# Performance work log

Hardware: AMD Instinct MI355X
Metric: run time of the kernel (lower is better)

The kernel has to match this reference:

```python
import jax, jax.numpy as jnp
import numpy as np

B, N, DIM = 2, 2048, 1024
H, DH = 16, 64
DIM_INNER = H * DH
EPS = float(jnp.finfo(jnp.float32).eps)  # torch nn.RMSNorm default eps = finfo.eps
THETA = 10000.0


def setup_inputs() -> dict:
    key = jax.random.key(0)
    ks = jax.random.split(key, 6)
    s = 0.02
    tokens = jax.random.normal(ks[0], (B, N, DIM), dtype=jnp.float32)
    w_norm = jnp.ones((DIM,), jnp.float32)                      # prenorm RMSNorm weight
    w_q = jax.random.normal(ks[1], (DIM, DIM_INNER), jnp.float32) * s
    w_k = jax.random.normal(ks[2], (DIM, 3 * DIM_INNER), jnp.float32) * s
    w_v = jax.random.normal(ks[3], (DIM, 3 * DIM_INNER), jnp.float32) * s
    w_key_norms = jnp.ones((3, DH), jnp.float32)                # 3 key RMSNorms
    w_nested_knorm = jnp.ones((DH,), jnp.float32)
    w_out = jax.random.normal(ks[4], (DIM_INNER, DIM), jnp.float32) * s
    return {"tokens": tokens, "w_norm": w_norm, "w_q": w_q, "w_k": w_k,
            "w_v": w_v, "w_key_norms": w_key_norms,
            "w_nested_knorm": w_nested_knorm, "w_out": w_out}


def rmsnorm(x, w):
    var = jnp.mean(jnp.square(x), axis=-1, keepdims=True)
    return x * jax.lax.rsqrt(var + EPS) * w


def rope(x):
    # interleaved (GPT-J style) rotary, as in rotary_embedding_torch defaults
    n, d = x.shape[-2], x.shape[-1]
    inv_freq = 1.0 / (THETA ** (jnp.arange(0, d, 2, dtype=jnp.float32) / d))
    freqs = jnp.arange(n, dtype=jnp.float32)[:, None] * inv_freq   # (n, d/2)
    cos = jnp.repeat(jnp.cos(freqs), 2, axis=-1)                   # (n, d)
    sin = jnp.repeat(jnp.sin(freqs), 2, axis=-1)
    x1, x2 = x[..., ::2], x[..., 1::2]
    x_rot = jnp.stack((-x2, x1), axis=-1).reshape(x.shape)         # rotate_half
    return x * cos + x_rot * sin


def attend(q, k, v):
    # rotate_queries_with_cached_keys with equal lengths -> plain rotary on both
    q = rope(q)
    k = rope(k)
    d = q.shape[-1]
    scores = jnp.einsum('bhqd,bhkd->bhqk', q, k) / jnp.sqrt(jnp.float32(d))
    n = scores.shape[-1]
    causal = jnp.tril(jnp.ones((n, n), dtype=bool))
    scores = jnp.where(causal, scores, -jnp.inf)
    attn = jax.nn.softmax(scores, axis=-1)
    return jnp.einsum('bhqk,bhkd->bhqd', attn, v)


def reference(tokens, w_norm, w_q, w_k, w_v, w_key_norms, w_nested_knorm, w_out):
    b, n = tokens.shape[:2]
    x = rmsnorm(tokens, w_norm)                                    # prenorm
    q = (x @ w_q).reshape(b, n, H, DH).transpose(0, 2, 1, 3)       # (b,h,n,d)
    # chunk(3, dim=-1) then split heads -> (3,b,h,n,d)
    ks = (x @ w_k).reshape(b, n, 3, H, DH).transpose(2, 0, 3, 1, 4)
    vs = (x @ w_v).reshape(b, n, 3, H, DH).transpose(2, 0, 3, 1, 4)
    ks = rmsnorm(ks, w_key_norms[:, None, None, None, :])          # per-branch key norm
    # three parallel causal attentions sharing the same queries
    nq, nk, nv = jax.vmap(attend, in_axes=(None, 0, 0))(q, ks, vs)
    nk = rmsnorm(nk, w_nested_knorm)
    out = attend(nq, nk, nv)                                       # nested attention
    out = out.transpose(0, 2, 1, 3).reshape(b, n, DIM_INNER)       # merge heads
    return out @ w_out
```

## Files before the change

kernel.cpp:

```cpp
#include <hip/hip_runtime.h>
#include <hip/hip_bf16.h>
#include <stdint.h>

typedef unsigned short u16;
typedef __attribute__((ext_vector_type(8))) short short8;
typedef __attribute__((ext_vector_type(4))) float float4v;
typedef __attribute__((ext_vector_type(4))) unsigned int uint4v;

#define B_    2
#define N_    2048
#define DIM_  1024
#define H_    16
#define DH_   64
#define DI_   1024
#define EPS_  1.1920928955078125e-07f
#define LOG2_THETA 13.287712379549449f
#define SCL_  0.18033688011112042f

__device__ __forceinline__ float bf2f(u16 u) {
    union { unsigned int i; float f; } v; v.i = ((unsigned int)u) << 16; return v.f;
}
__device__ __forceinline__ u16 f2bf(float f) {
    union { float f; unsigned int i; } v; v.f = f;
    unsigned int r = v.i + 0x7fff + ((v.i >> 16) & 1);
    return (u16)(r >> 16);
}
__device__ __forceinline__ unsigned int cvtpk(float a, float b) {
    unsigned int r;
    asm("v_cvt_pk_bf16_f32 %0, %1, %2" : "=v"(r) : "v"(a), "v"(b));
    return r;
}
__device__ __forceinline__ int perm32(int n) {
    return (n & ~31) + (((n >> 2) & 3) * 8) + (((n >> 4) & 1) * 4) + (n & 3);
}

__global__ __launch_bounds__(256) void k_pre(
    const float* __restrict__ w_q, const float* __restrict__ w_k,
    const float* __restrict__ w_v, u16* __restrict__ dstW,
    const float* __restrict__ tok, const float* __restrict__ w_norm,
    u16* __restrict__ xn) {
    int bx = blockIdx.x;
    int t = threadIdx.x;
    __shared__ float tile[32][33];
    __shared__ float red[4];
    if (bx < 7168) {
        int c0 = (bx % 224) * 32, k0 = (bx / 224) * 32;
        const float* src; int sN, sc0;
        if (c0 < 1024)      { src = w_q; sN = 1024; sc0 = c0; }
        else if (c0 < 4096) { src = w_k; sN = 3072; sc0 = c0 - 1024; }
        else                { src = w_v; sN = 3072; sc0 = c0 - 4096; }
        int tx = t & 31, ty = t >> 5;
#pragma unroll
        for (int i = 0; i < 4; ++i)
            tile[ty + 8 * i][tx] = src[(size_t)(k0 + ty + 8 * i) * sN + sc0 + tx];
        __syncthreads();
#pragma unroll
        for (int i = 0; i < 4; ++i)
            dstW[(size_t)(c0 + ty + 8 * i) * 1024 + k0 + tx] = f2bf(tile[tx][ty + 8 * i]);
    } else {
        int row = bx - 7168;
        const float* tr = tok + (size_t)row * DIM_ + t * 4;
        float4v v = *(const float4v*)tr;
        float ss = v[0] * v[0] + v[1] * v[1] + v[2] * v[2] + v[3] * v[3];
#pragma unroll
        for (int o = 32; o; o >>= 1) ss += __shfl_xor(ss, o, 64);
        if ((t & 63) == 0) red[t >> 6] = ss;
        __syncthreads();
        ss = red[0] + red[1] + red[2] + red[3];
        float rs = rsqrtf(ss * (1.0f / DIM_) + EPS_);
        const float* wp = w_norm + t * 4;
        uint2 pk;
        pk.x = cvtpk(v[0] * rs * wp[0], v[1] * rs * wp[1]);
        pk.y = cvtpk(v[2] * rs * wp[2], v[3] * rs * wp[3]);
        *(uint2*)(xn + (size_t)row * DIM_ + t * 4) = pk;
    }
}

__global__ __launch_bounds__(256) void k_transpose(
    const float* __restrict__ src, u16* __restrict__ dst, int K, int N) {
    __shared__ float tile[32][33];
    int n0 = blockIdx.x * 32, k0 = blockIdx.y * 32;
    int tx = threadIdx.x, ty = threadIdx.y;
#pragma unroll
    for (int i = 0; i < 4; ++i)
        tile[ty + 8 * i][tx] = src[(size_t)(k0 + ty + 8 * i) * N + n0 + tx];
    __syncthreads();
#pragma unroll
    for (int i = 0; i < 4; ++i)
        dst[(size_t)(n0 + ty + 8 * i) * K + k0 + tx] = f2bf(tile[tx][ty + 8 * i]);
}

__global__ __launch_bounds__(256) void k_post1(
    u16* __restrict__ QKVB, u16* __restrict__ Vt, const float* __restrict__ w) {
    int bx = blockIdx.x;
    int t = threadIdx.x;
    __shared__ u16 tile[64][72];
    if (bx < 3072) {
        int y = bx >> 5;
        int s = y >> 5;
        int b = (y >> 4) & 1;
        int h = y & 15;
        int n0 = (bx & 31) * 64;
#pragma unroll
        for (int i = 0; i < 2; ++i) {
            int idx = i * 256 + t;
            int row = idx >> 3, c = idx & 7;
            uint4v v = *(const uint4v*)(QKVB + ((size_t)(b * N_) + n0 + row) * 7168
                                            + 4096 + s * 1024 + h * 64 + c * 8);
            *(uint4v*)&tile[row][c * 8] = v;
        }
        __syncthreads();
        u16* out = Vt + (size_t)y * 64 * N_;
#pragma unroll
        for (int i = 0; i < 2; ++i) {
            int idx = i * 256 + t;
            int dh = idx >> 3, og = idx & 7;
            u16 vals[8];
#pragma unroll
            for (int j = 0; j < 8; ++j) {
                int m = og * 8 + j;
                int nn = (m & 32) + (m & 3) + ((m >> 3) & 3) * 4 + ((m >> 2) & 1) * 16;
                vals[j] = tile[nn][dh];
            }
            *(uint4v*)(out + (size_t)dh * N_ + n0 + og * 8) = *(const uint4v*)vals;
        }
    } else {
        int wid = (bx - 3072) * 4 + (t >> 6);
        int lane = t & 63;
        int r8 = lane >> 3, e8 = lane & 7;
        int hg = wid & 1;
        int s = (wid >> 1) % 3;
        int row = wid / 6;
        int n = row & (N_ - 1);
        int h = hg * 8 + r8;
        u16* p = QKVB + (size_t)row * 7168 + 1024 + s * 1024 + h * 64 + e8 * 8;
        uint4v v = *(const uint4v*)p;
        float x[8];
#pragma unroll
        for (int j = 0; j < 8; ++j) x[j] = bf2f(((const u16*)&v)[j]);
        float ss = 0.f;
#pragma unroll
        for (int j = 0; j < 8; ++j) ss += x[j] * x[j];
        ss += __shfl_xor(ss, 1, 64);
        ss += __shfl_xor(ss, 2, 64);
        ss += __shfl_xor(ss, 4, 64);
        float rs = rsqrtf(ss * (1.0f / 64.0f) + EPS_);
        const float* ws = w + s * 64 + e8 * 8;
        uint4v pk;
#pragma unroll
        for (int tp = 0; tp < 4; ++tp) {
            int d0 = e8 * 8 + 2 * tp;
            float xn0 = x[2 * tp] * rs * ws[2 * tp];
            float xn1 = x[2 * tp + 1] * rs * ws[2 * tp + 1];
            float inv = exp2f(-(float)d0 * (LOG2_THETA / 64.0f));
            float fr = (float)n * inv;
            float sv, cv;
            __sincosf(fr, &sv, &cv);
            pk[tp] = cvtpk(xn0 * cv - xn1 * sv, xn1 * cv + xn0 * sv);
        }
        *(uint4v*)p = pk;
    }
}

template <bool OUT_F32>
__global__ __launch_bounds__(256) void k_gemm_bt(
    const u16* __restrict__ A, const u16* __restrict__ Bt, void* __restrict__ Cv,
    int K, int Ncols) {
    __shared__ u16 As[2][128 * 32];
    __shared__ u16 Bs[2][128 * 32];
    int m0 = blockIdx.x * 128, n0 = blockIdx.y * 128;
    int t = threadIdx.x;
    int w = t >> 6, lane = t & 63, ln = lane & 15, quad = lane >> 4;
    int wm = w & 1, wn = w >> 1;
    float4v acc[4][4] = {};
    const u16* Ag = A + (size_t)m0 * K;
    const u16* Bg = Bt + (size_t)n0 * K;

    auto stage = [&](int k0, int buf) {
#pragma unroll
        for (int i = 0; i < 2; ++i) {
            int idx = i * 256 + t;
            int row = idx >> 2, kb = idx & 3;
            int csrc = (kb ^ ((row >> 1) & 3)) * 8;
            const u16* ga = Ag + (size_t)row * K + k0 + csrc;
            const u16* gb = Bg + (size_t)row * K + k0 + csrc;
            __builtin_amdgcn_global_load_lds(
                (const __attribute__((address_space(1))) void*)ga,
                (__attribute__((address_space(3))) void*)(As[buf] + idx * 8), 16, 0, 0);
            __builtin_amdgcn_global_load_lds(
                (const __attribute__((address_space(1))) void*)gb,
                (__attribute__((address_space(3))) void*)(Bs[buf] + idx * 8), 16, 0, 0);
        }
    };

    int nk = K >> 5;
    stage(0, 0);
    int rchunk = (quad ^ ((ln >> 1) & 3)) * 8;

    for (int kt = 0; kt < nk; ++kt) {
        asm volatile("s_waitcnt vmcnt(0)" ::: "memory");
        __syncthreads();
        if (kt + 1 < nk) stage((kt + 1) << 5, (kt + 1) & 1);
        int buf = kt & 1;
        short8 af[4], bfr[4];
#pragma unroll
        for (int mt = 0; mt < 4; ++mt)
            af[mt] = *(const short8*)(As[buf] + (wm * 64 + mt * 16 + ln) * 32 + rchunk);
#pragma unroll
        for (int nt = 0; nt < 4; ++nt)
            bfr[nt] = *(const short8*)(Bs[buf] + (wn * 64 + nt * 16 + ln) * 32 + rchunk);
#pragma unroll
        for (int mt = 0; mt < 4; ++mt)
#pragma unroll
            for (int nt = 0; nt < 4; ++nt)
                acc[mt][nt] = __builtin_amdgcn_mfma_f32_16x16x32_bf16(
                    af[mt], bfr[nt], acc[mt][nt], 0, 0, 0);
    }
#pragma unroll
    for (int mt = 0; mt < 4; ++mt)
#pragma unroll
        for (int nt = 0; nt < 4; ++nt)
#pragma unroll
            for (int r = 0; r < 4; ++r) {
                int row = m0 + wm * 64 + mt * 16 + quad * 4 + r;
                int col = n0 + wn * 64 + nt * 16 + ln;
                if (OUT_F32)
                    ((float*)Cv)[(size_t)row * Ncols + col] = acc[mt][nt][r];
                else
                    ((u16*)Cv)[(size_t)row * Ncols + col] = f2bf(acc[mt][nt][r]);
            }
}

__global__ __launch_bounds__(256, 3) void k_flash(
    const u16* __restrict__ Q, int q_stride,
    const u16* __restrict__ K, const u16* __restrict__ Vt,
    u16* __restrict__ O, u16* __restrict__ Ot,
    int kv_stride, int set_off, size_t o_set_stride,
    const float* __restrict__ wnk) {
    int bh = blockIdx.x;
    int qt = gridDim.y - 1 - blockIdx.y;
    int s = blockIdx.z;
    int b = bh >> 4, h = bh & 15;
    int t = threadIdx.x;
    int w = t >> 6, lane = t & 63, ln = lane & 15, quad = lane >> 4;
    int lnx = ln & 7;
    int q0 = qt * 128;
    int qw = q0 + w * 32;

    const u16* Qb  = Q + ((size_t)b * N_) * q_stride + h * 64;
    const u16* Kb  = K + ((size_t)b * N_) * kv_stride + (size_t)s * set_off + h * 64;
    const u16* Vtb = Vt + (size_t)((s * B_ + b) * H_ + h) * (64 * (size_t)N_);

    __shared__ u16 Ks[2][64][64];
    __shared__ u16 Vs[2][64][64];

    short8 ones;
#pragma unroll
    for (int j = 0; j < 8; ++j) ((u16*)&ones)[j] = 0x3F80;

    short8 qf[2][2];
    float mrow[2];
    float4v accO[2][4] = {};
    float4v accL[2] = {};
#pragma unroll
    for (int g = 0; g < 2; ++g) {
        int qg = qw + g * 16;
        int tokn = qg + ln;
        short8 raw[2];
#pragma unroll
        for (int f = 0; f < 2; ++f)
            raw[f] = *(const short8*)(Qb + (size_t)tokn * q_stride + f * 32 + quad * 8);
        float qn = 0.f;
#pragma unroll
        for (int f = 0; f < 2; ++f)
#pragma unroll
            for (int j = 0; j < 8; ++j) {
                float v = bf2f(((const u16*)&raw[f])[j]);
                qn += v * v;
            }
        qn += __shfl_xor(qn, 16, 64);
        qn += __shfl_xor(qn, 32, 64);
        mrow[g] = sqrtf(qn) * (8.0f * SCL_) * 1.03f + 1e-6f;
#pragma unroll
        for (int f = 0; f < 2; ++f) {
            u16 out8[8];
            int dbase = f * 32 + quad * 8;
#pragma unroll
            for (int tp = 0; tp < 4; ++tp) {
                int d = dbase + 2 * tp;
                float inv = exp2f((float)d * (-LOG2_THETA / 64.0f));
                float fr = (float)tokn * inv;
                float sv, cv;
                __sincosf(fr, &sv, &cv);
                float x0 = bf2f(((const u16*)&raw[f])[2 * tp]);
                float x1 = bf2f(((const u16*)&raw[f])[2 * tp + 1]);
                out8[2 * tp]     = f2bf((x0 * cv - x1 * sv) * SCL_);
                out8[2 * tp + 1] = f2bf((x1 * cv + x0 * sv) * SCL_);
            }
            qf[g][f] = *(const short8*)out8;
        }
    }

    int ntb = 2 * qt + 2;

    auto stage = [&](int kt0, int buf) {
        int k0 = kt0 * 64;
#pragma unroll
        for (int i = 0; i < 2; ++i) {
            int idx = i * 256 + t;
            int row = idx >> 3, c = idx & 7;
            int csrc = ((c ^ (row & 7)) * 8);
            const u16* ga = Kb + (size_t)(k0 + row) * kv_stride + csrc;
            __builtin_amdgcn_global_load_lds(
                (const __attribute__((address_space(1))) void*)ga,
                (__attribute__((address_space(3))) void*)&Ks[buf][row][c * 8], 16, 0, 0);
            const u16* gv = Vtb + (size_t)row * N_ + k0 + csrc;
            __builtin_amdgcn_global_load_lds(
                (const __attribute__((address_space(1))) void*)gv,
                (__attribute__((address_space(3))) void*)&Vs[buf][row][c * 8], 16, 0, 0);
        }
    };
    stage(0, 0);

    for (int kt0 = 0; kt0 < ntb; ++kt0) {
        asm volatile("s_waitcnt vmcnt(0)" ::: "memory");
        __syncthreads();
        if (kt0 + 1 < ntb) stage(kt0 + 1, (kt0 + 1) & 1);
        int buf = kt0 & 1;
        int k0 = kt0 * 64;
        if (k0 > qw + 31) continue;

        short8 kf[4][2];
#pragma unroll
        for (int kt = 0; kt < 4; ++kt) {
            const u16* krow = &Ks[buf][kt * 16 + ln][0];
            kf[kt][0] = *(const short8*)(krow + ((quad ^ lnx) * 8));
            kf[kt][1] = *(const short8*)(krow + (((4 + quad) ^ lnx) * 8));
        }

        short8 pb[2][2];
#pragma unroll
        for (int g = 0; g < 2; ++g) {
            int qg = qw + g * 16;
            float4v st[4];
#pragma unroll
            for (int kt = 0; kt < 4; ++kt) {
                float4v sa = {-mrow[g], -mrow[g], -mrow[g], -mrow[g]};
                sa = __builtin_amdgcn_mfma_f32_16x16x32_bf16(kf[kt][0], qf[g][0], sa, 0, 0, 0);
                sa = __builtin_amdgcn_mfma_f32_16x16x32_bf16(kf[kt][1], qf[g][1], sa, 0, 0, 0);
                st[kt] = sa;
            }
            if (k0 + 63 <= qg) {
#pragma unroll
                for (int c = 0; c < 2; ++c) {
                    uint4v pk;
#pragma unroll
                    for (int kt2 = 0; kt2 < 2; ++kt2) {
                        pk[kt2 * 2 + 0] = cvtpk(exp2f(st[c * 2 + kt2][0]),
                                                exp2f(st[c * 2 + kt2][1]));
                        pk[kt2 * 2 + 1] = cvtpk(exp2f(st[c * 2 + kt2][2]),
                                                exp2f(st[c * 2 + kt2][3]));
                    }
                    pb[g][c] = *(short8*)&pk;
                }
            } else {
                int qr = qg + ln;
#pragma unroll
                for (int c = 0; c < 2; ++c) {
                    uint4v pk;
#pragma unroll
                    for (int kt2 = 0; kt2 < 2; ++kt2) {
                        int kt = c * 2 + kt2;
                        float e[4];
#pragma unroll
                        for (int r = 0; r < 4; ++r) {
                            int kg = k0 + kt * 16 + quad * 4 + r;
                            float arg = (kg <= qr) ? st[kt][r] : -1e30f;
                            e[r] = exp2f(arg);
                        }
                        pk[kt2 * 2 + 0] = cvtpk(e[0], e[1]);
                        pk[kt2 * 2 + 1] = cvtpk(e[2], e[3]);
                    }
                    pb[g][c] = *(short8*)&pk;
                }
            }
        }

#pragma unroll
        for (int dc = 0; dc < 4; ++dc) {
            const u16* vrow = &Vs[buf][dc * 16 + ln][0];
            short8 vf0 = *(const short8*)(vrow + ((quad ^ lnx) * 8));
            short8 vf1 = *(const short8*)(vrow + (((4 + quad) ^ lnx) * 8));
#pragma unroll
            for (int g = 0; g < 2; ++g) {
                accO[g][dc] = __builtin_amdgcn_mfma_f32_16x16x32_bf16(vf0, pb[g][0], accO[g][dc], 0, 0, 0);
                accO[g][dc] = __builtin_amdgcn_mfma_f32_16x16x32_bf16(vf1, pb[g][1], accO[g][dc], 0, 0, 0);
            }
        }
#pragma unroll
        for (int g = 0; g < 2; ++g) {
            accL[g] = __builtin_amdgcn_mfma_f32_16x16x32_bf16(ones, pb[g][0], accL[g], 0, 0, 0);
            accL[g] = __builtin_amdgcn_mfma_f32_16x16x32_bf16(ones, pb[g][1], accL[g], 0, 0, 0);
        }
    }

#pragma unroll
    for (int g = 0; g < 2; ++g) {
        float rinv = 1.0f / accL[g][0];
        int qg = qw + g * 16;
        int qr = qg + ln;
        if (s == 2) {
            u16* Otb = Ot + (size_t)(b * H_ + h) * (64 * (size_t)N_);
            int pos = perm32(qr & (N_ - 1)) + (qr & ~(N_ - 1));
#pragma unroll
            for (int dc = 0; dc < 4; ++dc)
#pragma unroll
                for (int r = 0; r < 4; ++r)
                    Otb[(size_t)(dc * 16 + quad * 4 + r) * N_ + pos] =
                        f2bf(accO[g][dc][r] * rinv);
        } else if (wnk && s == 1) {
            u16* Ob = O + o_set_stride + ((size_t)b * N_) * DI_ + h * 64;
            float o[4][4];
            float ss = 0.f;
#pragma unroll
            for (int dc = 0; dc < 4; ++dc)
#pragma unroll
                for (int r = 0; r < 4; ++r) {
                    float x = accO[g][dc][r] * rinv;
                    o[dc][r] = x;
                    ss += x * x;
                }
            ss += __shfl_xor(ss, 16, 64);
            ss += __shfl_xor(ss, 32, 64);
            float rs2 = rsqrtf(ss * (1.0f / 64.0f) + EPS_);
#pragma unroll
            for (int dc = 0; dc < 4; ++dc) {
                uint2 pk;
#pragma unroll
                for (int rp = 0; rp < 2; ++rp) {
                    int d0 = dc * 16 + quad * 4 + 2 * rp;
                    float x0 = o[dc][2 * rp]     * rs2 * wnk[d0];
                    float x1 = o[dc][2 * rp + 1] * rs2 * wnk[d0 + 1];
                    float inv = exp2f(-(float)d0 * (LOG2_THETA / 64.0f));
                    float fr = (float)qr * inv;
                    float sv, cv;
                    __sincosf(fr, &sv, &cv);
                    unsigned int u = cvtpk(x0 * cv - x1 * sv, x1 * cv + x0 * sv);
                    if (rp == 0) pk.x = u; else pk.y = u;
                }
                *(uint2*)(Ob + (size_t)qr * DI_ + dc * 16 + quad * 4) = pk;
            }
        } else {
            u16* Ob = O + (size_t)s * o_set_stride + ((size_t)b * N_) * DI_ + h * 64;
#pragma unroll
            for (int dc = 0; dc < 4; ++dc) {
                uint2 pk;
                pk.x = cvtpk(accO[g][dc][0] * rinv, accO[g][dc][1] * rinv);
                pk.y = cvtpk(accO[g][dc][2] * rinv, accO[g][dc][3] * rinv);
                *(uint2*)(Ob + (size_t)qr * DI_ + dc * 16 + quad * 4) = pk;
            }
        }
    }
}

extern "C" void kernel_launch(void* const* d_in, const int* in_sizes, int n_in,
                              void* d_out, int out_size, void* d_ws, size_t ws_size,
                              hipStream_t stream) {
    const float* tok     = (const float*)d_in[0];
    const float* w_norm  = (const float*)d_in[1];
    const float* w_q     = (const float*)d_in[2];
    const float* w_k     = (const float*)d_in[3];
    const float* w_v     = (const float*)d_in[4];
    const float* w_keyn  = (const float*)d_in[5];
    const float* w_nestk = (const float*)d_in[6];
    const float* w_o     = (const float*)d_in[7];

    char* ws = (char*)d_ws;
    const size_t MB = 1024 * 1024;
    u16* QKVB  = (u16*)(ws + 0 * MB);
    u16* VtB   = (u16*)(ws + 56 * MB);
    u16* NQKV  = (u16*)(ws + 80 * MB);
    u16* WQKVT = (u16*)(ws + 80 * MB);
    u16* NVt   = (u16*)(ws + 96 * MB);
    u16* XN    = (u16*)(ws + 96 * MB);
    u16* OUT2  = (u16*)(ws + 104 * MB);
    u16* WOT   = (u16*)(ws + 80 * MB);

    const size_t SET = (size_t)B_ * N_ * DI_;

    k_pre<<<7168 + 4096, 256, 0, stream>>>(w_q, w_k, w_v, WQKVT, tok, w_norm, XN);

    k_gemm_bt<false><<<dim3(32, 56), 256, 0, stream>>>(XN, WQKVT, QKVB, 1024, 7168);

    k_post1<<<3072 + 6144, 256, 0, stream>>>(QKVB, VtB, w_keyn);

    k_flash<<<dim3(B_ * H_, N_ / 128, 3), 256, 0, stream>>>(
        QKVB, 7168, QKVB + 1024, VtB, NQKV, NVt, 7168, 1024, SET, w_nestk);

    k_flash<<<dim3(B_ * H_, N_ / 128, 1), 256, 0, stream>>>(
        NQKV, 1024, NQKV + SET, NVt, OUT2, NVt , 1024, 0, 0, nullptr);

    k_transpose<<<dim3(32, 32), dim3(32, 8), 0, stream>>>(w_o, WOT, 1024, 1024);
    k_gemm_bt<true><<<dim3(32, 8), 256, 0, stream>>>(OUT2, WOT, (float*)d_out, 1024, 1024);
}
```

Baseline: 368.2 us.

## Stage two KV tiles per barrier in flash kernel to halve sync count

The flash attention loop now loads a 128-key window (two 64-key sub-tiles) per double-buffered stage and computes both sub-tiles between barriers. This halves the number of vmcnt waits and __syncthreads per query tile. In exchange, LDS use doubles to 64KB per block, and launch bounds drop to 2 blocks per CU, which lowers occupancy and latency hiding.

```diff
diff --git a/kernel.cpp b/kernel.cpp
--- a/kernel.cpp
+++ b/kernel.cpp
@@ -231,7 +231,7 @@
             }
 }
 
-__global__ __launch_bounds__(256, 3) void k_flash(
+__global__ __launch_bounds__(256, 2) void k_flash(
     const u16* __restrict__ Q, int q_stride,
     const u16* __restrict__ K, const u16* __restrict__ Vt,
     u16* __restrict__ O, u16* __restrict__ Ot,
@@ -251,8 +251,8 @@
     const u16* Kb  = K + ((size_t)b * N_) * kv_stride + (size_t)s * set_off + h * 64;
     const u16* Vtb = Vt + (size_t)((s * B_ + b) * H_ + h) * (64 * (size_t)N_);
 
-    __shared__ u16 Ks[2][64][64];
-    __shared__ u16 Vs[2][64][64];
+    __shared__ u16 Ks[2][2][64][64];
+    __shared__ u16 Vs[2][2][64][64];
 
     short8 ones;
 #pragma unroll
@@ -302,42 +302,37 @@
     }
 
     int ntb = 2 * qt + 2;
-
-    auto stage = [&](int kt0, int buf) {
-        int k0 = kt0 * 64;
-#pragma unroll
-        for (int i = 0; i < 2; ++i) {
-            int idx = i * 256 + t;
-            int row = idx >> 3, c = idx & 7;
-            int csrc = ((c ^ (row & 7)) * 8);
-            const u16* ga = Kb + (size_t)(k0 + row) * kv_stride + csrc;
-            __builtin_amdgcn_global_load_lds(
-                (const __attribute__((address_space(1))) void*)ga,
-                (__attribute__((address_space(3))) void*)&Ks[buf][row][c * 8], 16, 0, 0);
-            const u16* gv = Vtb + (size_t)row * N_ + k0 + csrc;
-            __builtin_amdgcn_global_load_lds(
-                (const __attribute__((address_space(1))) void*)gv,
-                (__attribute__((address_space(3))) void*)&Vs[buf][row][c * 8], 16, 0, 0);
+    int nwin = ntb >> 1;
+
+    auto stage = [&](int win, int buf) {
+#pragma unroll
+        for (int sub = 0; sub < 2; ++sub) {
+            int k0 = (win * 2 + sub) * 64;
+#pragma unroll
+            for (int i = 0; i < 2; ++i) {
+                int idx = i * 256 + t;
+                int row = idx >> 3, c = idx & 7;
+                int csrc = ((c ^ (row & 7)) * 8);
+                const u16* ga = Kb + (size_t)(k0 + row) * kv_stride + csrc;
+                __builtin_amdgcn_global_load_lds(
+                    (const __attribute__((address_space(1))) void*)ga,
+                    (__attribute__((address_space(3))) void*)&Ks[buf][sub][row][c * 8], 16, 0, 0);
+                const u16* gv = Vtb + (size_t)row * N_ + k0 + csrc;
+                __builtin_amdgcn_global_load_lds(
+                    (const __attribute__((address_space(1))) void*)gv,
+                    (__attribute__((address_space(3))) void*)&Vs[buf][sub][row][c * 8], 16, 0, 0);
+            }
         }
     };
-    stage(0, 0);
-
-    for (int kt0 = 0; kt0 < ntb; ++kt0) {
-        asm volatile("s_waitcnt vmcnt(0)" ::: "memory");
-        __syncthreads();
-        if (kt0 + 1 < ntb) stage(kt0 + 1, (kt0 + 1) & 1);
-        int buf = kt0 & 1;
-        int k0 = kt0 * 64;
-        if (k0 > qw + 31) continue;
-
+
+    auto compute = [&](int buf, int sub, int k0) {
         short8 kf[4][2];
 #pragma unroll
         for (int kt = 0; kt < 4; ++kt) {
-            const u16* krow = &Ks[buf][kt * 16 + ln][0];
+            const u16* krow = &Ks[buf][sub][kt * 16 + ln][0];
             kf[kt][0] = *(const short8*)(krow + ((quad ^ lnx) * 8));
             kf[kt][1] = *(const short8*)(krow + (((4 + quad) ^ lnx) * 8));
         }
-
         short8 pb[2][2];
 #pragma unroll
         for (int g = 0; g < 2; ++g) {
@@ -385,10 +380,9 @@
                 }
             }
         }
-
 #pragma unroll
         for (int dc = 0; dc < 4; ++dc) {
-            const u16* vrow = &Vs[buf][dc * 16 + ln][0];
+            const u16* vrow = &Vs[buf][sub][dc * 16 + ln][0];
             short8 vf0 = *(const short8*)(vrow + ((quad ^ lnx) * 8));
             short8 vf1 = *(const short8*)(vrow + (((4 + quad) ^ lnx) * 8));
 #pragma unroll
@@ -402,6 +396,20 @@
             accL[g] = __builtin_amdgcn_mfma_f32_16x16x32_bf16(ones, pb[g][0], accL[g], 0, 0, 0);
             accL[g] = __builtin_amdgcn_mfma_f32_16x16x32_bf16(ones, pb[g][1], accL[g], 0, 0, 0);
         }
+    };
+
+    stage(0, 0);
+
+    for (int wv = 0; wv < nwin; ++wv) {
+        asm volatile("s_waitcnt vmcnt(0)" ::: "memory");
+        __syncthreads();
+        if (wv + 1 < nwin) stage(wv + 1, (wv + 1) & 1);
+        int buf = wv & 1;
+        int k0 = wv * 128;
+        if (k0 > qw + 31) continue;
+        compute(buf, 0, k0);
+        if (k0 + 64 <= qw + 31)
+            compute(buf, 1, k0 + 64);
     }
 
 #pragma unroll
```

Measured after the change: 367.1 us. About the same (-0.3%).
